# Optimization experiments

Hardware: AMD Instinct MI355X
Metric: run time of the kernel (lower is better)

## Reference

```python
import jax, jax.numpy as jnp
import numpy as np

B, T, C, H = 4, 2048, 1024, 16
D = C // H  # head_dim = 64


def setup_inputs() -> dict:
    key = jax.random.key(0)
    k1, k2, k3, k4 = jax.random.split(key, 4)
    x = jax.random.normal(k1, (B, T, C), dtype=jnp.float32)
    # realistic padding: each sequence has length in [T//2, T]
    lengths = jax.random.randint(k4, (B,), T // 2, T + 1)
    padding_mask = jnp.arange(T)[None, :] < lengths[:, None]  # True = keep
    # weights stored [in, out] (equivalent to torch Linear weight transposed)
    w_qkv = jax.random.normal(k2, (C, 3 * C), dtype=jnp.float32) * (C ** -0.5)
    w_out = jax.random.normal(k3, (C, C), dtype=jnp.float32) * (C ** -0.5)
    b_out = jnp.zeros((C,), dtype=jnp.float32)
    return {"x": x, "padding_mask": padding_mask, "w_qkv": w_qkv, "w_out": w_out, "b_out": b_out}


def reference(x, padding_mask, w_qkv, w_out, b_out):
    scale = D ** -0.5
    qkv = x @ w_qkv  # [B,T,3C]
    q, k, v = jnp.split(qkv, 3, axis=-1)

    def split_heads(t):
        return t.reshape(B, T, H, D).transpose(0, 2, 1, 3)  # [B,H,T,D]

    q, k, v = split_heads(q), split_heads(k), split_heads(v)
    attn = jnp.einsum("bhqd,bhkd->bhqk", q, k) * scale  # [B,H,T,T]
    mask = padding_mask[:, None, None, :]  # [B,1,1,T]
    attn = jnp.where(mask, attn, jnp.finfo(attn.dtype).min)
    attn = jax.nn.softmax(attn, axis=-1)
    # dropout is identity in eval mode
    out = jnp.einsum("bhqk,bhkd->bhqd", attn, v)  # [B,H,T,D]
    out = out.transpose(0, 2, 1, 3).reshape(B, T, C)
    return out @ w_out + b_out
```

## Files before the change

kernel.cpp:

```cpp
#include <hip/hip_runtime.h>
#include <hip/hip_bf16.h>

#define Bb 4
#define Tt 2048
#define Cc 1024
#define Hh 16

typedef unsigned short u16;
typedef __attribute__((ext_vector_type(8))) __bf16 bf16x8;
typedef __attribute__((ext_vector_type(4))) float  f32x4;

__device__ __forceinline__ u16 f2bf_hw(float f) {
    __bf16 h = (__bf16)f;
    return *(u16*)&h;
}

__device__ __forceinline__ unsigned cvt_pk_bf16(float a, float b) {
    unsigned r;
    asm("v_cvt_pk_bf16_f32 %0, %1, %2" : "=v"(r) : "v"(a), "v"(b));
    return r;
}

__device__ __forceinline__ float fexp2(float x) {
#if __has_builtin(__builtin_amdgcn_exp2f)
    return __builtin_amdgcn_exp2f(x);
#else
    return __expf(x * 0.6931471805599453f);
#endif
}

__device__ __forceinline__ void gld_lds16(const void* g, void* l) {
    __builtin_amdgcn_global_load_lds(
        (__attribute__((address_space(1))) void*)(g),
        (__attribute__((address_space(3))) void*)(l),
        16, 0, 0);
}

__device__ __forceinline__ f32x4 mfma16(bf16x8 a, bf16x8 b, f32x4 c) {
    return __builtin_amdgcn_mfma_f32_16x16x32_bf16(a, b, c, 0, 0, 0);
}

__global__ void cast_f32_bf16(const float* __restrict__ in, u16* __restrict__ out, int n4) {
    int i = blockIdx.x * 256 + threadIdx.x;
    if (i < n4) {
        float4 v = ((const float4*)in)[i];
        uint2 o;
        o.x = cvt_pk_bf16(v.x, v.y);
        o.y = cvt_pk_bf16(v.z, v.w);
        ((uint2*)out)[i] = o;
    }
}

__global__ void castT_f32_bf16(const float* __restrict__ in, u16* __restrict__ out,
                               int K, int N, int scaleN, float sv) {
    __shared__ float Ls[64][65];
    const int n0 = blockIdx.x * 64, k0 = blockIdx.y * 64;
    const int t = threadIdx.x;
    #pragma unroll
    for (int s = 0; s < 4; ++s) {
        int idx = t + 256 * s;
        int r   = idx >> 4;
        int c4  = (idx & 15) * 4;
        float4 v = *(const float4*)&in[(size_t)(k0 + r) * N + n0 + c4];
        Ls[r][c4 + 0] = v.x; Ls[r][c4 + 1] = v.y;
        Ls[r][c4 + 2] = v.z; Ls[r][c4 + 3] = v.w;
    }
    __syncthreads();
    #pragma unroll
    for (int s = 0; s < 2; ++s) {
        int idx = t + 256 * s;
        int n   = idx >> 3;
        int kc  = (idx & 7) * 8;
        const float sc = (n0 + n < scaleN) ? sv : 1.0f;
        alignas(16) u16 tmp[8];
        #pragma unroll
        for (int i = 0; i < 8; ++i) tmp[i] = f2bf_hw(Ls[kc + i][n] * sc);
        *(uint4*)&out[(size_t)(n0 + n) * K + k0 + kc] = *(const uint4*)tmp;
    }
}

__global__ void repack_frags(const u16* __restrict__ qkv,
                             u16* __restrict__ kx, u16* __restrict__ vx) {
    __shared__ u16 Kt[64 * 80];
    __shared__ u16 Vt[64 * 80];
    const int t = threadIdx.x;
    const int ch = blockIdx.x, bh = blockIdx.y, b = bh >> 4, h = bh & 15;
    const int kc = ch * 64;

    #pragma unroll
    for (int u = 0; u < 2; ++u) {
        int id = t + 256 * u;
        int key = id >> 3, c8 = id & 7;
        const size_t row = (size_t)(b * Tt + kc + key) * (3 * Cc) + h * 64 + c8 * 8;
        *(uint4*)&Kt[key * 80 + c8 * 8] = *(const uint4*)&qkv[row + Cc];
        *(uint4*)&Vt[key * 80 + c8 * 8] = *(const uint4*)&qkv[row + 2 * Cc];
    }
    __syncthreads();

    const size_t obase = (size_t)(bh * 32 + ch) * 4096;
    #pragma unroll
    for (int u = 0; u < 2; ++u) {
        int id = t + 256 * u;
        int lane = id & 63, ks = (id >> 6) & 1, jt = id >> 7;
        int l16 = lane & 15, quad = lane >> 4;
        uint4 kv = *(const uint4*)&Kt[(16 * jt + l16) * 80 + 32 * ks + quad * 8];
        *(uint4*)&kx[obase + (size_t)(jt * 2 + ks) * 512 + lane * 8] = kv;
        alignas(16) u16 tmp[8];
        #pragma unroll
        for (int j = 0; j < 8; ++j)
            tmp[j] = Vt[(32 * ks + quad * 8 + j) * 80 + 16 * jt + l16];
        *(uint4*)&vx[obase + (size_t)(jt * 2 + ks) * 512 + lane * 8] = *(const uint4*)tmp;
    }
}

__global__ __launch_bounds__(256, 3) void gemm_bt_bf16(
    const u16* __restrict__ A, const u16* __restrict__ Bt,
    const float* __restrict__ bias,
    u16* __restrict__ outB, float* __restrict__ outF,
    int M, int N, int K)
{
    __shared__ u16 As[128 * 32];
    __shared__ u16 Bs[128 * 32];
    const int t = threadIdx.x;
    const int w = t >> 6, lane = t & 63;
    const int quad = lane >> 4, l16 = lane & 15;
    const int wr = w >> 1, wc = w & 1;
    const int m0 = blockIdx.y * 128, n0 = blockIdx.x * 128;

    int aoff[4], boff[4];
    #pragma unroll
    for (int i = 0; i < 4; ++i) {
        int rA = 64 * wr + 16 * i + l16;
        aoff[i] = rA * 32 + ((quad ^ ((rA >> 1) & 3)) * 8);
        int rB = 64 * wc + 16 * i + l16;
        boff[i] = rB * 32 + ((quad ^ ((rB >> 1) & 3)) * 8);
    }

    f32x4 acc[4][4] = {};

    for (int k0 = 0; k0 < K; k0 += 32) {
        __syncthreads();
        #pragma unroll
        for (int u = 0; u < 2; ++u) {
            const int i   = 2 * w + u;
            const int row = 16 * i + (lane >> 2);
            const int c   = (lane & 3) ^ ((row >> 1) & 3);
            gld_lds16(A  + (size_t)(m0 + row) * K + k0 + c * 8, (void*)(As + i * 512 + lane * 8));
            gld_lds16(Bt + (size_t)(n0 + row) * K + k0 + c * 8, (void*)(Bs + i * 512 + lane * 8));
        }
        asm volatile("s_waitcnt vmcnt(0)" ::: "memory");
        __syncthreads();

        bf16x8 af[4], bfr[4];
        #pragma unroll
        for (int i = 0; i < 4; ++i) af[i]  = *(const bf16x8*)&As[aoff[i]];
        #pragma unroll
        for (int j = 0; j < 4; ++j) bfr[j] = *(const bf16x8*)&Bs[boff[j]];
        #pragma unroll
        for (int i = 0; i < 4; ++i)
            #pragma unroll
            for (int j = 0; j < 4; ++j)
                acc[i][j] = mfma16(af[i], bfr[j], acc[i][j]);
    }

    const int rbase = m0 + 64 * wr + quad * 4;
    const int cbase = n0 + 64 * wc + l16;
    if (outF) {
        float bv[4];
        #pragma unroll
        for (int j = 0; j < 4; ++j) bv[j] = bias[cbase + 16 * j];
        #pragma unroll
        for (int i = 0; i < 4; ++i)
            #pragma unroll
            for (int r = 0; r < 4; ++r) {
                size_t ro = (size_t)(rbase + 16 * i + r) * N;
                #pragma unroll
                for (int j = 0; j < 4; ++j)
                    outF[ro + cbase + 16 * j] = acc[i][j][r] + bv[j];
            }
    } else {
        #pragma unroll
        for (int i = 0; i < 4; ++i)
            #pragma unroll
            for (int r = 0; r < 4; ++r) {
                size_t ro = (size_t)(rbase + 16 * i + r) * N;
                #pragma unroll
                for (int j = 0; j < 4; ++j)
                    outB[ro + cbase + 16 * j] = f2bf_hw(acc[i][j][r]);
            }
    }
}

__global__ __launch_bounds__(256, 2) void attn_mfma4(
    const u16* __restrict__ qkv, const u16* __restrict__ kx, const u16* __restrict__ vx,
    const int* __restrict__ mask, u16* __restrict__ outO)
{
    __shared__ u16 KVs[8192];
    __shared__ u16 Pss[4][16 * 68];

    const int t = threadIdx.x;
    const int w = t >> 6, lane = t & 63;
    const int quad = lane >> 4, l16 = lane & 15;
    const int bh = blockIdx.x, qb = blockIdx.y, b = bh >> 4, h = bh & 15;

    int sum = 0;
    {
        const int4* mp = (const int4*)(mask + b * Tt) + lane * 8;
        #pragma unroll
        for (int i = 0; i < 8; ++i) { int4 m4 = mp[i]; sum += m4.x + m4.y + m4.z + m4.w; }
        #pragma unroll
        for (int off = 1; off < 64; off <<= 1) sum += __shfl_xor(sum, off);
    }
    const int L = sum;

    const int q0 = qb * 256 + w * 64;
    bf16x8 qf[4][2];
    #pragma unroll
    for (int qq = 0; qq < 4; ++qq) {
        const u16* qp = qkv + (size_t)(b * Tt + q0 + 16 * qq + l16) * (3 * Cc) + h * 64 + quad * 8;
        qf[qq][0] = *(const bf16x8*)(qp);
        qf[qq][1] = *(const bf16x8*)(qp + 32);
    }

    f32x4 oacc[4][4] = {};
    f32x4 lacc[4]    = {};
    const __bf16 onebf = (__bf16)1.0f;
    const bf16x8 ones  = {onebf, onebf, onebf, onebf, onebf, onebf, onebf, onebf};

    const int nfull = L >> 6;
    const int nch   = (L + 63) >> 6;
    const size_t cb0 = (size_t)bh * 32 * 4096;
    u16* Pw = Pss[w];

    {
        uint4 k0a = *(const uint4*)&kx[cb0 + t * 8];
        uint4 k0b = *(const uint4*)&kx[cb0 + 2048 + t * 8];
        uint4 v0a = *(const uint4*)&vx[cb0 + t * 8];
        uint4 v0b = *(const uint4*)&vx[cb0 + 2048 + t * 8];
        *(uint4*)&KVs[t * 8]        = k0a;
        *(uint4*)&KVs[2048 + t * 8] = k0b;
        *(uint4*)&KVs[4096 + t * 8] = v0a;
        *(uint4*)&KVs[6144 + t * 8] = v0b;
    }
    __syncthreads();

    for (int ch = 0; ch < nch; ++ch) {
        const int cc = (ch + 1 < nch) ? ch + 1 : ch;
        const size_t nb = cb0 + (size_t)cc * 4096;
        uint4 nk0 = *(const uint4*)&kx[nb + t * 8];
        uint4 nk1 = *(const uint4*)&kx[nb + 2048 + t * 8];
        uint4 nv0 = *(const uint4*)&vx[nb + t * 8];
        uint4 nv1 = *(const uint4*)&vx[nb + 2048 + t * 8];

        const u16* Kb = KVs;
        const u16* Vb = KVs + 4096;

        bf16x8 kf[4][2];
        #pragma unroll
        for (int jt = 0; jt < 4; ++jt)
            #pragma unroll
            for (int ks = 0; ks < 2; ++ks)
                kf[jt][ks] = *(const bf16x8*)&Kb[(jt * 2 + ks) * 512 + lane * 8];

        bf16x8 vf[4][2];
        #pragma unroll
        for (int dt = 0; dt < 4; ++dt)
            #pragma unroll
            for (int ks = 0; ks < 2; ++ks)
                vf[dt][ks] = *(const bf16x8*)&Vb[(dt * 2 + ks) * 512 + lane * 8];

        #pragma unroll
        for (int qq = 0; qq < 4; ++qq) {
            f32x4 st[4];
            #pragma unroll
            for (int jt = 0; jt < 4; ++jt) {
                f32x4 z = {0.f, 0.f, 0.f, 0.f};
                z = mfma16(kf[jt][0], qf[qq][0], z);
                st[jt] = mfma16(kf[jt][1], qf[qq][1], z);
            }
            uint2 pk[4];
            if (ch < nfull) {
                #pragma unroll
                for (int jt = 0; jt < 4; ++jt) {
                    pk[jt].x = cvt_pk_bf16(fexp2(st[jt][0]), fexp2(st[jt][1]));
                    pk[jt].y = cvt_pk_bf16(fexp2(st[jt][2]), fexp2(st[jt][3]));
                }
            } else {
                const int kc = ch * 64;
                #pragma unroll
                for (int jt = 0; jt < 4; ++jt) {
                    const int kb = kc + 16 * jt + quad * 4;
                    float e[4];
                    #pragma unroll
                    for (int r = 0; r < 4; ++r)
                        e[r] = (kb + r < L) ? fexp2(st[jt][r]) : 0.f;
                    pk[jt].x = cvt_pk_bf16(e[0], e[1]);
                    pk[jt].y = cvt_pk_bf16(e[2], e[3]);
                }
            }
            #pragma unroll
            for (int jt = 0; jt < 4; ++jt)
                *(uint2*)&Pw[l16 * 68 + 16 * jt + quad * 4] = pk[jt];

            #pragma unroll
            for (int ks = 0; ks < 2; ++ks) {
                const u16* pr = &Pw[l16 * 68 + 32 * ks + quad * 8];
                uint2 pa = *(const uint2*)pr;
                uint2 pb = *(const uint2*)(pr + 4);
                uint4 comb = {pa.x, pa.y, pb.x, pb.y};
                bf16x8 pf = *(const bf16x8*)&comb;
                #pragma unroll
                for (int dt = 0; dt < 4; ++dt)
                    oacc[qq][dt] = mfma16(pf, vf[dt][ks], oacc[qq][dt]);
                lacc[qq] = mfma16(pf, ones, lacc[qq]);
            }
        }

        __syncthreads();
        *(uint4*)&KVs[t * 8]        = nk0;
        *(uint4*)&KVs[2048 + t * 8] = nk1;
        *(uint4*)&KVs[4096 + t * 8] = nv0;
        *(uint4*)&KVs[6144 + t * 8] = nv1;
        __syncthreads();
    }

    #pragma unroll
    for (int qq = 0; qq < 4; ++qq)
        #pragma unroll
        for (int r = 0; r < 4; ++r) {
            const float inv = 1.f / lacc[qq][r];
            const size_t ro = (size_t)(b * Tt + q0 + 16 * qq + quad * 4 + r) * Cc + h * 64 + l16;
            #pragma unroll
            for (int dt = 0; dt < 4; ++dt)
                outO[ro + 16 * dt] = f2bf_hw(oacc[qq][dt][r] * inv);
        }
}

extern "C" void kernel_launch(void* const* d_in, const int* in_sizes, int n_in,
                              void* d_out, int out_size, void* d_ws, size_t ws_size,
                              hipStream_t stream) {
    const float* x     = (const float*)d_in[0];
    const int*   mask  = (const int*)  d_in[1];
    const float* w_qkv = (const float*)d_in[2];
    const float* w_out = (const float*)d_in[3];
    const float* b_out = (const float*)d_in[4];
    float*       outp  = (float*)d_out;

    const int M = Bb * Tt;
    char* ws = (char*)d_ws;
    u16* xb     = (u16*)(ws);
    u16* wqkvT  = (u16*)(ws + (16u << 20));
    u16* woutT  = (u16*)(ws + (22u << 20));
    u16* qkv    = (u16*)(ws + (24u << 20));
    u16* kx     = (u16*)(ws + (72u << 20));
    u16* vx     = (u16*)(ws + (88u << 20));
    u16* attnO  = (u16*)(ws);

    const float c2 = 0.18033688011112042f;

    cast_f32_bf16<<<(M * Cc / 4 + 255) / 256, 256, 0, stream>>>(x, xb, M * Cc / 4);
    castT_f32_bf16<<<dim3(3 * Cc / 64, Cc / 64), 256, 0, stream>>>(w_qkv, wqkvT, Cc, 3 * Cc, Cc, c2);
    castT_f32_bf16<<<dim3(Cc / 64, Cc / 64), 256, 0, stream>>>(w_out, woutT, Cc, Cc, 0, 1.0f);

    gemm_bt_bf16<<<dim3(3 * Cc / 128, M / 128), 256, 0, stream>>>(
        xb, wqkvT, nullptr, qkv, nullptr, M, 3 * Cc, Cc);

    repack_frags<<<dim3(Tt / 64, Bb * Hh), 256, 0, stream>>>(qkv, kx, vx);

    attn_mfma4<<<dim3(Bb * Hh, Tt / 256), 256, 0, stream>>>(qkv, kx, vx, mask, attnO);

    gemm_bt_bf16<<<dim3(Cc / 128, M / 128), 256, 0, stream>>>(
        attnO, woutT, b_out, nullptr, outp, M, Cc, Cc);
}
```

Baseline: 268.6 us.

## Fuse K/V fragment repack into QKV GEMM epilogue, drop repack kernel

Adds a QKV-specific GEMM whose epilogue writes Q to a compact buffer and scatters K and V straight into the MFMA fragment layout the attention kernel expects. This removes the separate repack kernel, along with its extra read and write of K/V and one launch. The cost is scattered 2-byte global stores in the epilogue, which coalesce worse than the original row-major writes. Attention now reads Q with a stride of C instead of 3C.

```diff
diff --git a/kernel.cpp b/kernel.cpp
--- a/kernel.cpp
+++ b/kernel.cpp
@@ -76,40 +76,6 @@
         #pragma unroll
         for (int i = 0; i < 8; ++i) tmp[i] = f2bf_hw(Ls[kc + i][n] * sc);
         *(uint4*)&out[(size_t)(n0 + n) * K + k0 + kc] = *(const uint4*)tmp;
-    }
-}
-
-__global__ void repack_frags(const u16* __restrict__ qkv,
-                             u16* __restrict__ kx, u16* __restrict__ vx) {
-    __shared__ u16 Kt[64 * 80];
-    __shared__ u16 Vt[64 * 80];
-    const int t = threadIdx.x;
-    const int ch = blockIdx.x, bh = blockIdx.y, b = bh >> 4, h = bh & 15;
-    const int kc = ch * 64;
-
-    #pragma unroll
-    for (int u = 0; u < 2; ++u) {
-        int id = t + 256 * u;
-        int key = id >> 3, c8 = id & 7;
-        const size_t row = (size_t)(b * Tt + kc + key) * (3 * Cc) + h * 64 + c8 * 8;
-        *(uint4*)&Kt[key * 80 + c8 * 8] = *(const uint4*)&qkv[row + Cc];
-        *(uint4*)&Vt[key * 80 + c8 * 8] = *(const uint4*)&qkv[row + 2 * Cc];
-    }
-    __syncthreads();
-
-    const size_t obase = (size_t)(bh * 32 + ch) * 4096;
-    #pragma unroll
-    for (int u = 0; u < 2; ++u) {
-        int id = t + 256 * u;
-        int lane = id & 63, ks = (id >> 6) & 1, jt = id >> 7;
-        int l16 = lane & 15, quad = lane >> 4;
-        uint4 kv = *(const uint4*)&Kt[(16 * jt + l16) * 80 + 32 * ks + quad * 8];
-        *(uint4*)&kx[obase + (size_t)(jt * 2 + ks) * 512 + lane * 8] = kv;
-        alignas(16) u16 tmp[8];
-        #pragma unroll
-        for (int j = 0; j < 8; ++j)
-            tmp[j] = Vt[(32 * ks + quad * 8 + j) * 80 + 16 * jt + l16];
-        *(uint4*)&vx[obase + (size_t)(jt * 2 + ks) * 512 + lane * 8] = *(const uint4*)tmp;
     }
 }
 
@@ -191,8 +157,116 @@
     }
 }
 
+__global__ __launch_bounds__(256, 3) void gemm_qkv_bt(
+    const u16* __restrict__ A, const u16* __restrict__ Bt,
+    u16* __restrict__ outQ, u16* __restrict__ kx, u16* __restrict__ vx)
+{
+    const int M = Bb * Tt, N = 3 * Cc, K = Cc;
+    __shared__ u16 As[128 * 32];
+    __shared__ u16 Bs[128 * 32];
+    const int t = threadIdx.x;
+    const int w = t >> 6, lane = t & 63;
+    const int quad = lane >> 4, l16 = lane & 15;
+    const int wr = w >> 1, wc = w & 1;
+    const int m0 = blockIdx.y * 128, n0 = blockIdx.x * 128;
+    (void)M; (void)N;
+
+    int aoff[4], boff[4];
+    #pragma unroll
+    for (int i = 0; i < 4; ++i) {
+        int rA = 64 * wr + 16 * i + l16;
+        aoff[i] = rA * 32 + ((quad ^ ((rA >> 1) & 3)) * 8);
+        int rB = 64 * wc + 16 * i + l16;
+        boff[i] = rB * 32 + ((quad ^ ((rB >> 1) & 3)) * 8);
+    }
+
+    f32x4 acc[4][4] = {};
+
+    for (int k0 = 0; k0 < K; k0 += 32) {
+        __syncthreads();
+        #pragma unroll
+        for (int u = 0; u < 2; ++u) {
+            const int i   = 2 * w + u;
+            const int row = 16 * i + (lane >> 2);
+            const int c   = (lane & 3) ^ ((row >> 1) & 3);
+            gld_lds16(A  + (size_t)(m0 + row) * K + k0 + c * 8, (void*)(As + i * 512 + lane * 8));
+            gld_lds16(Bt + (size_t)(n0 + row) * K + k0 + c * 8, (void*)(Bs + i * 512 + lane * 8));
+        }
+        asm volatile("s_waitcnt vmcnt(0)" ::: "memory");
+        __syncthreads();
+
+        bf16x8 af[4], bfr[4];
+        #pragma unroll
+        for (int i = 0; i < 4; ++i) af[i]  = *(const bf16x8*)&As[aoff[i]];
+        #pragma unroll
+        for (int j = 0; j < 4; ++j) bfr[j] = *(const bf16x8*)&Bs[boff[j]];
+        #pragma unroll
+        for (int i = 0; i < 4; ++i)
+            #pragma unroll
+            for (int j = 0; j < 4; ++j)
+                acc[i][j] = mfma16(af[i], bfr[j], acc[i][j]);
+    }
+
+    const int rbase = m0 + 64 * wr + quad * 4;
+    const int cbase = n0 + 64 * wc + l16;
+    const int region = n0 >> 10;
+
+    if (region == 0) {
+        #pragma unroll
+        for (int i = 0; i < 4; ++i)
+            #pragma unroll
+            for (int r = 0; r < 4; ++r) {
+                size_t ro = (size_t)(rbase + 16 * i + r) * Cc;
+                #pragma unroll
+                for (int j = 0; j < 4; ++j)
+                    outQ[ro + cbase + 16 * j] = f2bf_hw(acc[i][j][r]);
+            }
+    } else if (region == 1) {
+        int colK[4];
+        #pragma unroll
+        for (int j = 0; j < 4; ++j) {
+            const int c = (cbase - 1024) + 16 * j;
+            const int h = c >> 6, d = c & 63;
+            colK[j] = h * 131072 + (d >> 5) * 512 + ((d >> 3) & 3) * 128 + (d & 7);
+        }
+        #pragma unroll
+        for (int i = 0; i < 4; ++i)
+            #pragma unroll
+            for (int r = 0; r < 4; ++r) {
+                const int row = rbase + 16 * i + r;
+                const int b = row >> 11, key = row & 2047;
+                const int ch = key >> 6, keyr = key & 63;
+                const int rowK = b * 2097152 + ch * 4096 + (keyr >> 4) * 1024 + (keyr & 15) * 8;
+                #pragma unroll
+                for (int j = 0; j < 4; ++j)
+                    kx[rowK + colK[j]] = f2bf_hw(acc[i][j][r]);
+            }
+    } else {
+        int colV[4];
+        #pragma unroll
+        for (int j = 0; j < 4; ++j) {
+            const int c = (cbase - 2048) + 16 * j;
+            const int h = c >> 6, d = c & 63;
+            colV[j] = h * 131072 + (d >> 4) * 1024 + (d & 15) * 8;
+        }
+        #pragma unroll
+        for (int i = 0; i < 4; ++i)
+            #pragma unroll
+            for (int r = 0; r < 4; ++r) {
+                const int row = rbase + 16 * i + r;
+                const int b = row >> 11, key = row & 2047;
+                const int ch = key >> 6, keyr = key & 63;
+                const int rowV = b * 2097152 + ch * 4096 + (keyr >> 5) * 512
+                               + ((keyr >> 3) & 3) * 128 + (keyr & 7);
+                #pragma unroll
+                for (int j = 0; j < 4; ++j)
+                    vx[rowV + colV[j]] = f2bf_hw(acc[i][j][r]);
+            }
+    }
+}
+
 __global__ __launch_bounds__(256, 2) void attn_mfma4(
-    const u16* __restrict__ qkv, const u16* __restrict__ kx, const u16* __restrict__ vx,
+    const u16* __restrict__ qb, const u16* __restrict__ kx, const u16* __restrict__ vx,
     const int* __restrict__ mask, u16* __restrict__ outO)
 {
     __shared__ u16 KVs[8192];
@@ -201,7 +275,7 @@
     const int t = threadIdx.x;
     const int w = t >> 6, lane = t & 63;
     const int quad = lane >> 4, l16 = lane & 15;
-    const int bh = blockIdx.x, qb = blockIdx.y, b = bh >> 4, h = bh & 15;
+    const int bh = blockIdx.x, qblk = blockIdx.y, b = bh >> 4, h = bh & 15;
 
     int sum = 0;
     {
@@ -213,11 +287,11 @@
     }
     const int L = sum;
 
-    const int q0 = qb * 256 + w * 64;
+    const int q0 = qblk * 256 + w * 64;
     bf16x8 qf[4][2];
     #pragma unroll
     for (int qq = 0; qq < 4; ++qq) {
-        const u16* qp = qkv + (size_t)(b * Tt + q0 + 16 * qq + l16) * (3 * Cc) + h * 64 + quad * 8;
+        const u16* qp = qb + (size_t)(b * Tt + q0 + 16 * qq + l16) * Cc + h * 64 + quad * 8;
         qf[qq][0] = *(const bf16x8*)(qp);
         qf[qq][1] = *(const bf16x8*)(qp + 32);
     }
@@ -351,9 +425,9 @@
     u16* xb     = (u16*)(ws);
     u16* wqkvT  = (u16*)(ws + (16u << 20));
     u16* woutT  = (u16*)(ws + (22u << 20));
-    u16* qkv    = (u16*)(ws + (24u << 20));
-    u16* kx     = (u16*)(ws + (72u << 20));
-    u16* vx     = (u16*)(ws + (88u << 20));
+    u16* qbuf   = (u16*)(ws + (24u << 20));
+    u16* kx     = (u16*)(ws + (40u << 20));
+    u16* vx     = (u16*)(ws + (56u << 20));
     u16* attnO  = (u16*)(ws);
 
     const float c2 = 0.18033688011112042f;
@@ -362,12 +436,10 @@
     castT_f32_bf16<<<dim3(3 * Cc / 64, Cc / 64), 256, 0, stream>>>(w_qkv, wqkvT, Cc, 3 * Cc, Cc, c2);
     castT_f32_bf16<<<dim3(Cc / 64, Cc / 64), 256, 0, stream>>>(w_out, woutT, Cc, Cc, 0, 1.0f);
 
-    gemm_bt_bf16<<<dim3(3 * Cc / 128, M / 128), 256, 0, stream>>>(
-        xb, wqkvT, nullptr, qkv, nullptr, M, 3 * Cc, Cc);
-
-    repack_frags<<<dim3(Tt / 64, Bb * Hh), 256, 0, stream>>>(qkv, kx, vx);
-
-    attn_mfma4<<<dim3(Bb * Hh, Tt / 256), 256, 0, stream>>>(qkv, kx, vx, mask, attnO);
+    gemm_qkv_bt<<<dim3(3 * Cc / 128, M / 128), 256, 0, stream>>>(
+        xb, wqkvT, qbuf, kx, vx);
+
+    attn_mfma4<<<dim3(Bb * Hh, Tt / 256), 256, 0, stream>>>(qbuf, kx, vx, mask, attnO);
 
     gemm_bt_bf16<<<dim3(Cc / 128, M / 128), 256, 0, stream>>>(
         attnO, woutT, b_out, nullptr, outp, M, Cc, Cc);
```

Result: faster. 260.9 us (-2.9%).
